# Kernel tuning notes

Measured on AMD Instinct MI355X. Metric: run time of the kernel, lower is better.

Reference implementation:

```python
import jax, jax.numpy as jnp
import numpy as np

T, B, M, H, NH = 4, 8, 1024, 768, 12
HD = H // NH
KMAX = 10


def _ln(x, s, b):
    mu = x.mean(-1, keepdims=True)
    var = ((x - mu) ** 2).mean(-1, keepdims=True)
    return (x - mu) * jax.lax.rsqrt(var + 1e-5) * s + b


def setup_inputs() -> dict:
    key = jax.random.key(0)
    ks = jax.random.split(key, 10)
    init = lambda k, shp: jax.random.normal(k, shp, jnp.float32) * 0.02
    return {
        'x': jax.random.normal(ks[0], (B, M, H), jnp.float32),
        'overlap': jax.random.randint(ks[1], (B, M, M), 0, KMAX + 1, jnp.int32),
        'lp': -jax.random.uniform(ks[2], (B, M), jnp.float32) * 10.0,
        'ln1_s': jnp.ones((T, H)), 'ln1_b': jnp.zeros((T, H)),
        'Wqkv': init(ks[3], (T, H, 3 * H)),
        'Wout': init(ks[4], (T, H, H)), 'bout': jnp.zeros((T, H)),
        'ln2_s': jnp.ones((T, H)), 'ln2_b': jnp.zeros((T, H)),
        'W1': init(ks[5], (T, H, 4 * H)), 'b1': jnp.zeros((T, 4 * H)),
        'W2': init(ks[6], (T, 4 * H, H)), 'b2': jnp.zeros((T, H)),
        'lno_s': jnp.ones((H,)), 'lno_b': jnp.zeros((H,)),
        'ov_emb': init(ks[7], (KMAX + 1,)),
        'ht_alpha': jnp.ones((1,), jnp.float32),
    }


def reference(x, overlap, lp, ln1_s, ln1_b, Wqkv, Wout, bout, ln2_s, ln2_b,
              W1, b1, W2, b2, lno_s, lno_b, ov_emb, ht_alpha):
    lp_c = jnp.clip(lp, -30.0, 0.0)                      # [B,M]
    ov = ov_emb[jnp.minimum(overlap, KMAX)]              # [B,M,M]
    bias = (ov - ht_alpha[0] * lp_c[:, None, :])[:, None]  # [B,1,M,M]
    scale = 1.0 / jnp.sqrt(jnp.float32(HD))
    for t in range(T):
        r = _ln(x, ln1_s[t], ln1_b[t])
        q, k, v = jnp.split(r @ Wqkv[t], 3, axis=-1)
        q = q.reshape(B, M, NH, HD).transpose(0, 2, 1, 3)
        k = k.reshape(B, M, NH, HD).transpose(0, 2, 1, 3)
        v = v.reshape(B, M, NH, HD).transpose(0, 2, 1, 3)
        s = jnp.einsum('bhqd,bhkd->bhqk', q, k) * scale + bias
        a = jax.nn.softmax(s, axis=-1)
        o = jnp.einsum('bhqk,bhkd->bhqd', a, v).transpose(0, 2, 1, 3).reshape(B, M, H)
        x = x + o @ Wout[t] + bout[t]
        h = _ln(x, ln2_s[t], ln2_b[t])
        x = x + jax.nn.gelu(h @ W1[t] + b1[t], approximate=False) @ W2[t] + b2[t]
    x = _ln(x, lno_s, lno_b)
    w = jax.nn.softmax(-lp_c, axis=1)                    # HT weights over m tokens
    return jnp.einsum('bm,bmh->bh', w, x)
```

## Files before the change

kernel.cpp:

```cpp
#include <hip/hip_runtime.h>
#include <hip/hip_bf16.h>
#include <math.h>

#define TT 4
#define BB 8
#define MM 1024
#define HH 768
#define NHEAD 12
#define HDIM 64
#define NTOK 8192
#define H3 2304
#define H4 3072

typedef __attribute__((ext_vector_type(8))) short bf16x8;
typedef __attribute__((ext_vector_type(4))) float f32x4;
typedef __attribute__((ext_vector_type(4))) unsigned short u16x4;

#define GLOBAL_AS(p) ((const __attribute__((address_space(1))) void*)(p))
#define LDS_AS(p)    ((__attribute__((address_space(3))) void*)(p))

__device__ __forceinline__ unsigned short f2bf(float f) {
  union { float f; unsigned u; } v; v.f = f;
  unsigned r = v.u + 0x7fffu + ((v.u >> 16) & 1u);
  return (unsigned short)(r >> 16);
}

__device__ __forceinline__ float fast_exp2(float x) {
#if __has_builtin(__builtin_amdgcn_exp2f)
  return __builtin_amdgcn_exp2f(x);
#else
  return exp2f(x);
#endif
}

__device__ __forceinline__ f32x4 mfma16(bf16x8 a, bf16x8 b, f32x4 c) {
  return __builtin_amdgcn_mfma_f32_16x16x32_bf16(a, b, c, 0, 0, 0);
}

__device__ __forceinline__ float block_sum256(float v, float* sh) {
  #pragma unroll
  for (int off = 32; off > 0; off >>= 1) v += __shfl_down(v, off);
  if ((threadIdx.x & 63) == 0) sh[threadIdx.x >> 6] = v;
  __syncthreads();
  v = sh[0] + sh[1] + sh[2] + sh[3];
  __syncthreads();
  return v;
}

__device__ __forceinline__ float block_max256(float v, float* sh) {
  #pragma unroll
  for (int off = 32; off > 0; off >>= 1) v = fmaxf(v, __shfl_down(v, off));
  if ((threadIdx.x & 63) == 0) sh[threadIdx.x >> 6] = v;
  __syncthreads();
  v = fmaxf(fmaxf(sh[0], sh[1]), fmaxf(sh[2], sh[3]));
  __syncthreads();
  return v;
}

__global__ __launch_bounds__(256) void wconv_kernel(const float* __restrict__ W,
                                                    unsigned short* __restrict__ Wt,
                                                    int K, int N) {
  __shared__ float tile[32][33];
  const int n0 = blockIdx.x * 32, k0 = blockIdx.y * 32;
  const int tx = threadIdx.x, ty = threadIdx.y;
  #pragma unroll
  for (int j = 0; j < 4; j++)
    tile[ty + j*8][tx] = W[(size_t)(k0 + ty + j*8) * N + n0 + tx];
  __syncthreads();
  #pragma unroll
  for (int j = 0; j < 4; j++)
    Wt[(size_t)(n0 + ty + j*8) * K + k0 + tx] = f2bf(tile[tx][ty + j*8]);
}

__global__ __launch_bounds__(256) void ln_kernel(const float* __restrict__ x,
                                                 const float* __restrict__ s,
                                                 const float* __restrict__ b,
                                                 unsigned short* __restrict__ out) {
  __shared__ float sh[4];
  const int row = blockIdx.x;
  const int tid = threadIdx.x;
  const float* xr = x + (size_t)row * HH;
  float v[3];
  float sum = 0.f;
  #pragma unroll
  for (int j = 0; j < 3; j++) { v[j] = xr[tid + j*256]; sum += v[j]; }
  sum = block_sum256(sum, sh);
  const float mu = sum * (1.f/768.f);
  float ss = 0.f;
  #pragma unroll
  for (int j = 0; j < 3; j++) { float d = v[j] - mu; ss += d*d; }
  ss = block_sum256(ss, sh);
  const float rstd = rsqrtf(ss * (1.f/768.f) + 1e-5f);
  #pragma unroll
  for (int j = 0; j < 3; j++) {
    int col = tid + j*256;
    out[(size_t)row * HH + col] = f2bf((v[j]-mu)*rstd*s[col] + b[col]);
  }
}

template<int EPI>
__global__ __launch_bounds__(256) void gemm_kernel(const unsigned short* __restrict__ A,
                                                   const unsigned short* __restrict__ Bt,
                                                   unsigned short* __restrict__ outB,
                                                   float* __restrict__ outF,
                                                   const float* __restrict__ bias,
                                                   int Ng, int Kg, int nx) {
  __shared__ unsigned short a_lds[2][128*64];
  __shared__ unsigned short b_lds[2][128*64];
  const int tid = threadIdx.x;
  const int w = tid >> 6, l = tid & 63;
  const int nwg = gridDim.x;
  const int lin = blockIdx.x;
  const int L = (lin & 7) * (nwg >> 3) + (lin >> 3);
  const int m0 = (L / nx) * 128, n0 = (L % nx) * 128;

  const int wr = (w >> 1) * 64, wc = (w & 1) * 64;
  const int l15 = l & 15, lhi = l >> 4;
  const int srow = w*32 + (l >> 3);
  const int schunk = (l & 7) ^ (l >> 3);
  const int scol = schunk << 3;

  f32x4 acc[4][4] = {};
  const int nk = Kg >> 6;
  int cur = 0;

  #pragma unroll
  for (int i = 0; i < 4; i++) {
    const unsigned short* gsa = A  + (size_t)(m0 + srow + i*8)*Kg + scol;
    const unsigned short* gsb = Bt + (size_t)(n0 + srow + i*8)*Kg + scol;
    __builtin_amdgcn_global_load_lds(GLOBAL_AS(gsa), LDS_AS(&a_lds[0][w*2048 + i*512]), 16, 0, 0);
    __builtin_amdgcn_global_load_lds(GLOBAL_AS(gsb), LDS_AS(&b_lds[0][w*2048 + i*512]), 16, 0, 0);
  }
  __syncthreads();

  for (int t = 0; t < nk; t++) {
    if (t + 1 < nk) {
      const int ks = (t + 1) << 6;
      #pragma unroll
      for (int i = 0; i < 4; i++) {
        const unsigned short* gsa = A  + (size_t)(m0 + srow + i*8)*Kg + ks + scol;
        const unsigned short* gsb = Bt + (size_t)(n0 + srow + i*8)*Kg + ks + scol;
        __builtin_amdgcn_global_load_lds(GLOBAL_AS(gsa), LDS_AS(&a_lds[cur^1][w*2048 + i*512]), 16, 0, 0);
        __builtin_amdgcn_global_load_lds(GLOBAL_AS(gsb), LDS_AS(&b_lds[cur^1][w*2048 + i*512]), 16, 0, 0);
      }
    }
    const unsigned short* ab = &a_lds[cur][0];
    const unsigned short* bb = &b_lds[cur][0];
    #pragma unroll
    for (int kb = 0; kb < 2; kb++) {
      bf16x8 af[4], bfr[4];
      const int rc = (kb*4 + lhi) ^ (l15 & 7);
      #pragma unroll
      for (int rb = 0; rb < 4; rb++)
        af[rb] = *(const bf16x8*)&ab[(wr + rb*16 + l15)*64 + (rc << 3)];
      #pragma unroll
      for (int nb = 0; nb < 4; nb++)
        bfr[nb] = *(const bf16x8*)&bb[(wc + nb*16 + l15)*64 + (rc << 3)];
      #pragma unroll
      for (int rb = 0; rb < 4; rb++)
        #pragma unroll
        for (int nb = 0; nb < 4; nb++)
          acc[rb][nb] = mfma16(af[rb], bfr[nb], acc[rb][nb]);
    }
    __syncthreads();
    cur ^= 1;
  }

  const int lr = lhi << 2;
  #pragma unroll
  for (int rb = 0; rb < 4; rb++)
    #pragma unroll
    for (int nb = 0; nb < 4; nb++) {
      const int row = m0 + wr + rb*16 + lr;
      const int col = n0 + wc + nb*16 + l15;
      #pragma unroll
      for (int r = 0; r < 4; r++) {
        float v = acc[rb][nb][r];
        const size_t off = (size_t)(row + r)*Ng + col;
        if (EPI == 0) {
          outB[off] = f2bf(v);
        } else if (EPI == 1) {
          v += bias[col];
          v = 0.5f * v * (1.f + erff(v * 0.70710678118654752f));
          outB[off] = f2bf(v);
        } else {
          v += bias[col] + outF[off];
          outF[off] = v;
        }
      }
    }
}

__global__ __launch_bounds__(256) void biasprep_kernel(const int* __restrict__ overlap,
                                                       const float* __restrict__ lp,
                                                       const float* __restrict__ ov_emb,
                                                       const float* __restrict__ ht_alpha,
                                                       float* __restrict__ biasP) {
  __shared__ float oe[11];
  if (threadIdx.x < 11) oe[threadIdx.x] = ov_emb[threadIdx.x] * 1.44269504088896f;
  __syncthreads();
  const float aL = ht_alpha[0] * 1.44269504088896f;
  const size_t base = ((size_t)blockIdx.x * 256 + threadIdx.x) * 4;
  const int b = (int)(base >> 20);
  const int k0 = (int)(base & 1023);
  int4 ov = *(const int4*)&overlap[base];
  float4 lv = *(const float4*)&lp[b * MM + k0];
  float4 o4;
  {
    int t0 = ov.x < 10 ? ov.x : 10; float c0 = fminf(fmaxf(lv.x, -30.f), 0.f); o4.x = oe[t0] - aL*c0;
    int t1 = ov.y < 10 ? ov.y : 10; float c1 = fminf(fmaxf(lv.y, -30.f), 0.f); o4.y = oe[t1] - aL*c1;
    int t2 = ov.z < 10 ? ov.z : 10; float c2 = fminf(fmaxf(lv.z, -30.f), 0.f); o4.z = oe[t2] - aL*c2;
    int t3 = ov.w < 10 ? ov.w : 10; float c3 = fminf(fmaxf(lv.w, -30.f), 0.f); o4.w = oe[t3] - aL*c3;
  }
  *(float4*)&biasP[base] = o4;
}

__global__ __launch_bounds__(256) void attn_kernel(const unsigned short* __restrict__ qkv,
                                                   const float* __restrict__ biasP,
                                                   unsigned short* __restrict__ obuf) {
  __shared__ unsigned short k_lds[64*64];
  __shared__ unsigned short v_lds[64*64];
  __shared__ unsigned short pmat[4][32*64];

  const int tid = threadIdx.x;
  const int w = tid >> 6, l = tid & 63;
  const int lin = blockIdx.x;
  const int L = (lin & 7) * 96 + (lin >> 3);
  const int h = L % 12;
  const int qb = (L / 12) & 7;
  const int b = L / 96;
  const int q0w = qb*128 + w*32;
  const int l15 = l & 15, lhi = l >> 4;
  const float SC = 0.125f * 1.44269504088896f;

  bf16x8 qf[2][2];
  #pragma unroll
  for (int rb = 0; rb < 2; rb++)
    #pragma unroll
    for (int kb = 0; kb < 2; kb++)
      qf[rb][kb] = *(const bf16x8*)&qkv[(size_t)(b*MM + q0w + rb*16 + l15)*H3 + h*HDIM + kb*32 + lhi*8];

  const float* brow[2];
  #pragma unroll
  for (int rb = 0; rb < 2; rb++)
    brow[rb] = biasP + (size_t)(b*MM + q0w + rb*16 + l15) * MM;

  f32x4 oacc[4][2] = {};
  float mrow[2] = {-INFINITY, -INFINITY};
  float lrow[2] = {0.f, 0.f};

  for (int kt = 0; kt < 16; kt++) {
    const int kbase = kt * 64;
    #pragma unroll
    for (int i = 0; i < 2; i++) {
      int idx = i*256 + tid;
      int kr = idx >> 3;
      int dc = (idx & 7) << 3;
      const size_t rowoff = (size_t)(b*MM + kbase + kr)*H3 + h*HDIM + dc;
      bf16x8 kv = *(const bf16x8*)&qkv[rowoff + HH];
      bf16x8 vv = *(const bf16x8*)&qkv[rowoff + 2*HH];
      *(bf16x8*)&k_lds[kr*64 + (dc ^ ((kr & 7) << 3))] = kv;
      #pragma unroll
      for (int j = 0; j < 8; j++) {
        int key = ((((dc >> 3) & 7) ^ j) & 7) << 3;
        v_lds[(dc + j)*64 + (kr ^ key)] = (unsigned short)(short)vv[j];
      }
    }
    __syncthreads();

    f32x4 sacc[4][2] = {};
    #pragma unroll
    for (int kb = 0; kb < 2; kb++) {
      bf16x8 ak[4];
      #pragma unroll
      for (int nb = 0; nb < 4; nb++) {
        int n = nb*16 + l15;
        ak[nb] = *(const bf16x8*)&k_lds[n*64 + ((kb*32 + lhi*8) ^ ((n & 7) << 3))];
      }
      #pragma unroll
      for (int nb = 0; nb < 4; nb++)
        #pragma unroll
        for (int rb = 0; rb < 2; rb++)
          sacc[nb][rb] = mfma16(ak[nb], qf[rb][kb], sacc[nb][rb]);
    }

    #pragma unroll
    for (int nb = 0; nb < 4; nb++)
      #pragma unroll
      for (int rb = 0; rb < 2; rb++) {
        f32x4 b4 = *(const f32x4*)&brow[rb][kbase + nb*16 + lhi*4];
        #pragma unroll
        for (int r = 0; r < 4; r++)
          sacc[nb][rb][r] = fmaf(sacc[nb][rb][r], SC, b4[r]);
      }

    float corrf[2];
    #pragma unroll
    for (int rb = 0; rb < 2; rb++) {
      float pm = sacc[0][rb][0];
      #pragma unroll
      for (int nb = 0; nb < 4; nb++)
        #pragma unroll
        for (int r = 0; r < 4; r++)
          pm = fmaxf(pm, sacc[nb][rb][r]);
      pm = fmaxf(pm, __shfl_xor(pm, 16));
      pm = fmaxf(pm, __shfl_xor(pm, 32));
      const float mnew = fmaxf(mrow[rb], pm);
      const float corr = fast_exp2(mrow[rb] - mnew);
      float rs = 0.f;
      #pragma unroll
      for (int nb = 0; nb < 4; nb++)
        #pragma unroll
        for (int r = 0; r < 4; r++) {
          float p = fast_exp2(sacc[nb][rb][r] - mnew);
          sacc[nb][rb][r] = p;
          rs += p;
        }
      rs += __shfl_xor(rs, 16);
      rs += __shfl_xor(rs, 32);
      mrow[rb] = mnew;
      lrow[rb] = lrow[rb]*corr + rs;
      corrf[rb] = corr;
    }
    #pragma unroll
    for (int db = 0; db < 4; db++)
      #pragma unroll
      for (int rb = 0; rb < 2; rb++)
        #pragma unroll
        for (int r = 0; r < 4; r++)
          oacc[db][rb][r] *= corrf[rb];

    unsigned short* pw = &pmat[w][0];
    #pragma unroll
    for (int nb = 0; nb < 4; nb++)
      #pragma unroll
      for (int rb = 0; rb < 2; rb++) {
        u16x4 pk;
        #pragma unroll
        for (int r = 0; r < 4; r++) pk[r] = f2bf(sacc[nb][rb][r]);
        *(u16x4*)&pw[(rb*16 + l15)*64 + ((nb*16 + lhi*4) ^ ((l15 & 7) << 3))] = pk;
      }

    #pragma unroll
    for (int kb = 0; kb < 2; kb++) {
      bf16x8 pb[2];
      #pragma unroll
      for (int rb = 0; rb < 2; rb++)
        pb[rb] = *(const bf16x8*)&pw[(rb*16 + l15)*64 + ((kb*32 + lhi*8) ^ ((l15 & 7) << 3))];
      bf16x8 av[4];
      #pragma unroll
      for (int db = 0; db < 4; db++) {
        int d = db*16 + l15;
        int key = ((((d >> 3) & 7) ^ (d & 7)) & 7) << 3;
        av[db] = *(const bf16x8*)&v_lds[d*64 + ((kb*32 + lhi*8) ^ key)];
      }
      #pragma unroll
      for (int db = 0; db < 4; db++)
        #pragma unroll
        for (int rb = 0; rb < 2; rb++)
          oacc[db][rb] = mfma16(av[db], pb[rb], oacc[db][rb]);
    }
    __syncthreads();
  }

  float inv[2] = { 1.f / lrow[0], 1.f / lrow[1] };
  unsigned short* pw = &pmat[w][0];
  #pragma unroll
  for (int db = 0; db < 4; db++)
    #pragma unroll
    for (int rb = 0; rb < 2; rb++) {
      u16x4 pk;
      #pragma unroll
      for (int r = 0; r < 4; r++) pk[r] = f2bf(oacc[db][rb][r] * inv[rb]);
      *(u16x4*)&pw[(rb*16 + l15)*64 + ((db*16 + lhi*4) ^ ((l15 & 7) << 3))] = pk;
    }
  #pragma unroll
  for (int rep = 0; rep < 4; rep++) {
    int qq = rep*8 + (l >> 3);
    int d0 = (l & 7) << 3;
    bf16x8 vv = *(const bf16x8*)&pw[qq*64 + (d0 ^ ((qq & 7) << 3))];
    *(bf16x8*)&obuf[(size_t)(b*MM + q0w + qq)*HH + h*HDIM + d0] = vv;
  }
}

__global__ __launch_bounds__(256) void htw_kernel(const float* __restrict__ lp,
                                                  float* __restrict__ w_ht) {
  __shared__ float sh[4];
  const int b = blockIdx.x, tid = threadIdx.x;
  float vals[4];
  float mx = -INFINITY;
  #pragma unroll
  for (int j = 0; j < 4; j++) {
    float lv = lp[b*MM + tid + j*256];
    float lc = fminf(fmaxf(lv, -30.f), 0.f);
    vals[j] = -lc;
    mx = fmaxf(mx, vals[j]);
  }
  mx = block_max256(mx, sh);
  float se = 0.f;
  #pragma unroll
  for (int j = 0; j < 4; j++) { vals[j] = expf(vals[j] - mx); se += vals[j]; }
  se = block_sum256(se, sh);
  const float inv = 1.f / se;
  #pragma unroll
  for (int j = 0; j < 4; j++) w_ht[b*MM + tid + j*256] = vals[j] * inv;
}

__global__ __launch_bounds__(256) void final_partial_kernel(const float* __restrict__ xbuf,
                                                            const float* __restrict__ lno_s,
                                                            const float* __restrict__ lno_b,
                                                            const float* __restrict__ w_ht,
                                                            float* __restrict__ part) {
  __shared__ float sh[4];
  const int b = blockIdx.x >> 4;
  const int chunk = blockIdx.x & 15;
  const int tid = threadIdx.x;
  float acc[3] = {0.f, 0.f, 0.f};
  float sc[3], bc[3];
  #pragma unroll
  for (int j = 0; j < 3; j++) { sc[j] = lno_s[tid + j*256]; bc[j] = lno_b[tid + j*256]; }
  for (int rr = 0; rr < 64; rr++) {
    const int tok = b*MM + chunk*64 + rr;
    const float* xr = xbuf + (size_t)tok * HH;
    float v[3]; float sum = 0.f;
    #pragma unroll
    for (int j = 0; j < 3; j++) { v[j] = xr[tid + j*256]; sum += v[j]; }
    sum = block_sum256(sum, sh);
    const float mu = sum * (1.f/768.f);
    float ss = 0.f;
    #pragma unroll
    for (int j = 0; j < 3; j++) { float d = v[j] - mu; ss += d*d; }
    ss = block_sum256(ss, sh);
    const float rstd = rsqrtf(ss * (1.f/768.f) + 1e-5f);
    const float wgt = w_ht[b*MM + chunk*64 + rr];
    #pragma unroll
    for (int j = 0; j < 3; j++) acc[j] += wgt * ((v[j]-mu)*rstd*sc[j] + bc[j]);
  }
  #pragma unroll
  for (int j = 0; j < 3; j++) part[(size_t)blockIdx.x * HH + tid + j*256] = acc[j];
}

__global__ __launch_bounds__(256) void final_reduce_kernel(const float* __restrict__ part,
                                                           float* __restrict__ out) {
  const int b = blockIdx.x;
  const int col = blockIdx.y*256 + threadIdx.x;
  float s = 0.f;
  #pragma unroll
  for (int c = 0; c < 16; c++) s += part[(size_t)(b*16 + c) * HH + col];
  out[b*HH + col] = s;
}

extern "C" void kernel_launch(void* const* d_in, const int* in_sizes, int n_in,
                              void* d_out, int out_size, void* d_ws, size_t ws_size,
                              hipStream_t stream) {
  (void)in_sizes; (void)n_in; (void)ws_size;
  const float* x      = (const float*)d_in[0];
  const int*   overlap= (const int*)d_in[1];
  const float* lp     = (const float*)d_in[2];
  const float* ln1_s  = (const float*)d_in[3];
  const float* ln1_b  = (const float*)d_in[4];
  const float* Wqkv   = (const float*)d_in[5];
  const float* Wout   = (const float*)d_in[6];
  const float* bout   = (const float*)d_in[7];
  const float* ln2_s  = (const float*)d_in[8];
  const float* ln2_b  = (const float*)d_in[9];
  const float* W1     = (const float*)d_in[10];
  const float* b1     = (const float*)d_in[11];
  const float* W2     = (const float*)d_in[12];
  const float* b2     = (const float*)d_in[13];
  const float* lno_s  = (const float*)d_in[14];
  const float* lno_b  = (const float*)d_in[15];
  const float* ov_emb = (const float*)d_in[16];
  const float* ht_alpha = (const float*)d_in[17];
  float* out = (float*)d_out;

  char* ws = (char*)d_ws;
  float*          xbuf  = (float*)(ws + 0);
  unsigned short* lnout = (unsigned short*)(ws + 25165824);
  unsigned short* qkv   = (unsigned short*)(ws + 37748736);
  unsigned short* obuf  = (unsigned short*)(ws + 75497472);
  unsigned short* gbuf  = (unsigned short*)(ws + 88080384);
  unsigned short* wbuf  = (unsigned short*)(ws + 138412032);
  float*          w_ht  = (float*)(ws + 143130624);
  float*          part  = (float*)(ws + 143163392);
  float*          biasP = (float*)gbuf;

  hipMemcpyAsync(xbuf, x, (size_t)NTOK * HH * sizeof(float), hipMemcpyDeviceToDevice, stream);
  htw_kernel<<<BB, 256, 0, stream>>>(lp, w_ht);

  for (int t = 0; t < TT; t++) {
    wconv_kernel<<<dim3(H3/32, HH/32), dim3(32, 8), 0, stream>>>(Wqkv + (size_t)t*HH*H3, wbuf, HH, H3);
    ln_kernel<<<NTOK, 256, 0, stream>>>(xbuf, ln1_s + t*HH, ln1_b + t*HH, lnout);
    gemm_kernel<0><<<(H3/128)*(NTOK/128), 256, 0, stream>>>(lnout, wbuf, qkv, nullptr, nullptr, H3, HH, H3/128);
    biasprep_kernel<<<(BB*MM*MM/4)/256, 256, 0, stream>>>(overlap, lp, ov_emb, ht_alpha, biasP);
    attn_kernel<<<BB*NHEAD*(MM/128), 256, 0, stream>>>(qkv, biasP, obuf);
    wconv_kernel<<<dim3(HH/32, HH/32), dim3(32, 8), 0, stream>>>(Wout + (size_t)t*HH*HH, wbuf, HH, HH);
    gemm_kernel<2><<<(HH/128)*(NTOK/128), 256, 0, stream>>>(obuf, wbuf, nullptr, xbuf, bout + t*HH, HH, HH, HH/128);
    ln_kernel<<<NTOK, 256, 0, stream>>>(xbuf, ln2_s + t*HH, ln2_b + t*HH, lnout);
    wconv_kernel<<<dim3(H4/32, HH/32), dim3(32, 8), 0, stream>>>(W1 + (size_t)t*HH*H4, wbuf, HH, H4);
    gemm_kernel<1><<<(H4/128)*(NTOK/128), 256, 0, stream>>>(lnout, wbuf, gbuf, nullptr, b1 + t*H4, H4, HH, H4/128);
    wconv_kernel<<<dim3(HH/32, H4/32), dim3(32, 8), 0, stream>>>(W2 + (size_t)t*H4*HH, wbuf, H4, HH);
    gemm_kernel<2><<<(HH/128)*(NTOK/128), 256, 0, stream>>>(gbuf, wbuf, nullptr, xbuf, b2 + t*HH, HH, H4, HH/128);
  }

  final_partial_kernel<<<BB*16, 256, 0, stream>>>(xbuf, lno_s, lno_b, w_ht, part);
  final_reduce_kernel<<<dim3(BB, 3), 256, 0, stream>>>(part, out);

  (void)out_size;
}
```

Before: 1.504 ms.

## Double-buffer attention K/V, defer softmax rescale, tanh GELU, hoist bias prep

Attention now double-buffers K/V in LDS, prefetching the next tile (K via direct global-to-LDS loads) while the current tile computes, and raises wave priority around the MFMA blocks. It also skips the output rescale when the running max grows by at most 8, the exact-erf GELU becomes a tanh approximation built on exp2, and the attention bias is built once in spare workspace instead of once per layer. Together these target load latency in attention, transcendental cost in the FC1 epilogue, and three redundant bias passes, at the cost of more LDS, an extra barrier per tile, and a GELU that differs slightly from the exact-erf reference.

```diff
diff --git a/kernel.cpp b/kernel.cpp
--- a/kernel.cpp
+++ b/kernel.cpp
@@ -181,7 +181,11 @@
           outB[off] = f2bf(v);
         } else if (EPI == 1) {
           v += bias[col];
-          v = 0.5f * v * (1.f + erff(v * 0.70710678118654752f));
+          float u = 0.79788456080287f * v * (1.f + 0.044715f * v * v);
+          u = fminf(u, 15.f);
+          float e = fast_exp2(u * 2.88539008177793f);
+          float th = 1.f - 2.f / (e + 1.f);
+          v = 0.5f * v * (1.f + th);
           outB[off] = f2bf(v);
         } else {
           v += bias[col] + outF[off];
@@ -218,8 +222,8 @@
 __global__ __launch_bounds__(256) void attn_kernel(const unsigned short* __restrict__ qkv,
                                                    const float* __restrict__ biasP,
                                                    unsigned short* __restrict__ obuf) {
-  __shared__ unsigned short k_lds[64*64];
-  __shared__ unsigned short v_lds[64*64];
+  __shared__ unsigned short k_lds[2][64*64];
+  __shared__ unsigned short v_lds[2][64*64];
   __shared__ unsigned short pmat[4][32*64];
 
   const int tid = threadIdx.x;
@@ -233,6 +237,10 @@
   const int l15 = l & 15, lhi = l >> 4;
   const float SC = 0.125f * 1.44269504088896f;
 
+  const int kr_s = l >> 3;
+  const int schunk = (l & 7) ^ kr_s;
+  const int dc = (l & 7) << 3;
+
   bf16x8 qf[2][2];
   #pragma unroll
   for (int rb = 0; rb < 2; rb++)
@@ -249,33 +257,55 @@
   float mrow[2] = {-INFINITY, -INFINITY};
   float lrow[2] = {0.f, 0.f};
 
+
+  {
+    #pragma unroll
+    for (int i = 0; i < 2; i++) {
+      const unsigned short* g = qkv + (size_t)(b*MM + 0 + i*32 + w*8 + kr_s)*H3 + h*HDIM + HH + schunk*8;
+      __builtin_amdgcn_global_load_lds(GLOBAL_AS(g), LDS_AS(&k_lds[0][(i*32 + w*8)*64]), 16, 0, 0);
+    }
+    bf16x8 vr[2];
+    #pragma unroll
+    for (int i = 0; i < 2; i++)
+      vr[i] = *(const bf16x8*)&qkv[(size_t)(b*MM + 0 + i*32 + w*8 + kr_s)*H3 + h*HDIM + 2*HH + dc];
+    #pragma unroll
+    for (int i = 0; i < 2; i++) {
+      int kr = i*32 + w*8 + kr_s;
+      #pragma unroll
+      for (int j = 0; j < 8; j++) {
+        int key = ((((dc >> 3) & 7) ^ j) & 7) << 3;
+        v_lds[0][(dc + j)*64 + (kr ^ key)] = (unsigned short)(short)vr[i][j];
+      }
+    }
+    __syncthreads();
+  }
+
+  int cur = 0;
   for (int kt = 0; kt < 16; kt++) {
     const int kbase = kt * 64;
-    #pragma unroll
-    for (int i = 0; i < 2; i++) {
-      int idx = i*256 + tid;
-      int kr = idx >> 3;
-      int dc = (idx & 7) << 3;
-      const size_t rowoff = (size_t)(b*MM + kbase + kr)*H3 + h*HDIM + dc;
-      bf16x8 kv = *(const bf16x8*)&qkv[rowoff + HH];
-      bf16x8 vv = *(const bf16x8*)&qkv[rowoff + 2*HH];
-      *(bf16x8*)&k_lds[kr*64 + (dc ^ ((kr & 7) << 3))] = kv;
-      #pragma unroll
-      for (int j = 0; j < 8; j++) {
-        int key = ((((dc >> 3) & 7) ^ j) & 7) << 3;
-        v_lds[(dc + j)*64 + (kr ^ key)] = (unsigned short)(short)vv[j];
-      }
-    }
-    __syncthreads();
+    bf16x8 vrN[2];
+    if (kt < 15) {
+      const int nbase = kbase + 64;
+      #pragma unroll
+      for (int i = 0; i < 2; i++) {
+        const unsigned short* g = qkv + (size_t)(b*MM + nbase + i*32 + w*8 + kr_s)*H3 + h*HDIM + HH + schunk*8;
+        __builtin_amdgcn_global_load_lds(GLOBAL_AS(g), LDS_AS(&k_lds[cur^1][(i*32 + w*8)*64]), 16, 0, 0);
+      }
+      #pragma unroll
+      for (int i = 0; i < 2; i++)
+        vrN[i] = *(const bf16x8*)&qkv[(size_t)(b*MM + nbase + i*32 + w*8 + kr_s)*H3 + h*HDIM + 2*HH + dc];
+    }
 
     f32x4 sacc[4][2] = {};
+    const unsigned short* kb_lds = &k_lds[cur][0];
+    __builtin_amdgcn_s_setprio(1);
     #pragma unroll
     for (int kb = 0; kb < 2; kb++) {
       bf16x8 ak[4];
       #pragma unroll
       for (int nb = 0; nb < 4; nb++) {
         int n = nb*16 + l15;
-        ak[nb] = *(const bf16x8*)&k_lds[n*64 + ((kb*32 + lhi*8) ^ ((n & 7) << 3))];
+        ak[nb] = *(const bf16x8*)&kb_lds[n*64 + ((kb*32 + lhi*8) ^ ((n & 7) << 3))];
       }
       #pragma unroll
       for (int nb = 0; nb < 4; nb++)
@@ -283,6 +313,7 @@
         for (int rb = 0; rb < 2; rb++)
           sacc[nb][rb] = mfma16(ak[nb], qf[rb][kb], sacc[nb][rb]);
     }
+    __builtin_amdgcn_s_setprio(0);
 
     #pragma unroll
     for (int nb = 0; nb < 4; nb++)
@@ -295,6 +326,7 @@
       }
 
     float corrf[2];
+    int defer[2];
     #pragma unroll
     for (int rb = 0; rb < 2; rb++) {
       float pm = sacc[0][rb][0];
@@ -305,8 +337,9 @@
           pm = fmaxf(pm, sacc[nb][rb][r]);
       pm = fmaxf(pm, __shfl_xor(pm, 16));
       pm = fmaxf(pm, __shfl_xor(pm, 32));
-      const float mnew = fmaxf(mrow[rb], pm);
-      const float corr = fast_exp2(mrow[rb] - mnew);
+      defer[rb] = __all(pm - mrow[rb] <= 8.0f);
+      const float mnew = defer[rb] ? mrow[rb] : fmaxf(mrow[rb], pm);
+      const float corr = defer[rb] ? 1.0f : fast_exp2(mrow[rb] - mnew);
       float rs = 0.f;
       #pragma unroll
       for (int nb = 0; nb < 4; nb++)
@@ -323,12 +356,14 @@
       corrf[rb] = corr;
     }
     #pragma unroll
-    for (int db = 0; db < 4; db++)
-      #pragma unroll
-      for (int rb = 0; rb < 2; rb++)
-        #pragma unroll
-        for (int r = 0; r < 4; r++)
-          oacc[db][rb][r] *= corrf[rb];
+    for (int rb = 0; rb < 2; rb++)
+      if (!defer[rb]) {
+        #pragma unroll
+        for (int db = 0; db < 4; db++)
+          #pragma unroll
+          for (int r = 0; r < 4; r++)
+            oacc[db][rb][r] *= corrf[rb];
+      }
 
     unsigned short* pw = &pmat[w][0];
     #pragma unroll
@@ -341,6 +376,8 @@
         *(u16x4*)&pw[(rb*16 + l15)*64 + ((nb*16 + lhi*4) ^ ((l15 & 7) << 3))] = pk;
       }
 
+    const unsigned short* vb_lds = &v_lds[cur][0];
+    __builtin_amdgcn_s_setprio(1);
     #pragma unroll
     for (int kb = 0; kb < 2; kb++) {
       bf16x8 pb[2];
@@ -352,7 +389,7 @@
       for (int db = 0; db < 4; db++) {
         int d = db*16 + l15;
         int key = ((((d >> 3) & 7) ^ (d & 7)) & 7) << 3;
-        av[db] = *(const bf16x8*)&v_lds[d*64 + ((kb*32 + lhi*8) ^ key)];
+        av[db] = *(const bf16x8*)&vb_lds[d*64 + ((kb*32 + lhi*8) ^ key)];
       }
       #pragma unroll
       for (int db = 0; db < 4; db++)
@@ -360,7 +397,22 @@
         for (int rb = 0; rb < 2; rb++)
           oacc[db][rb] = mfma16(av[db], pb[rb], oacc[db][rb]);
     }
+    __builtin_amdgcn_s_setprio(0);
+
     __syncthreads();
+    if (kt < 15) {
+      #pragma unroll
+      for (int i = 0; i < 2; i++) {
+        int kr = i*32 + w*8 + kr_s;
+        #pragma unroll
+        for (int j = 0; j < 8; j++) {
+          int key = ((((dc >> 3) & 7) ^ j) & 7) << 3;
+          v_lds[cur^1][(dc + j)*64 + (kr ^ key)] = (unsigned short)(short)vrN[i][j];
+        }
+      }
+    }
+    __syncthreads();
+    cur ^= 1;
   }
 
   float inv[2] = { 1.f / lrow[0], 1.f / lrow[1] };
@@ -453,7 +505,7 @@
 extern "C" void kernel_launch(void* const* d_in, const int* in_sizes, int n_in,
                               void* d_out, int out_size, void* d_ws, size_t ws_size,
                               hipStream_t stream) {
-  (void)in_sizes; (void)n_in; (void)ws_size;
+  (void)in_sizes; (void)n_in;
   const float* x      = (const float*)d_in[0];
   const int*   overlap= (const int*)d_in[1];
   const float* lp     = (const float*)d_in[2];
@@ -483,16 +535,20 @@
   unsigned short* wbuf  = (unsigned short*)(ws + 138412032);
   float*          w_ht  = (float*)(ws + 143130624);
   float*          part  = (float*)(ws + 143163392);
-  float*          biasP = (float*)gbuf;
+  const int prep_once = (ws_size >= (size_t)143556608 + (size_t)33554432);
+  float*          biasP = prep_once ? (float*)(ws + 143556608) : (float*)gbuf;
 
   hipMemcpyAsync(xbuf, x, (size_t)NTOK * HH * sizeof(float), hipMemcpyDeviceToDevice, stream);
   htw_kernel<<<BB, 256, 0, stream>>>(lp, w_ht);
+  if (prep_once)
+    biasprep_kernel<<<(BB*MM*MM/4)/256, 256, 0, stream>>>(overlap, lp, ov_emb, ht_alpha, biasP);
 
   for (int t = 0; t < TT; t++) {
     wconv_kernel<<<dim3(H3/32, HH/32), dim3(32, 8), 0, stream>>>(Wqkv + (size_t)t*HH*H3, wbuf, HH, H3);
     ln_kernel<<<NTOK, 256, 0, stream>>>(xbuf, ln1_s + t*HH, ln1_b + t*HH, lnout);
     gemm_kernel<0><<<(H3/128)*(NTOK/128), 256, 0, stream>>>(lnout, wbuf, qkv, nullptr, nullptr, H3, HH, H3/128);
-    biasprep_kernel<<<(BB*MM*MM/4)/256, 256, 0, stream>>>(overlap, lp, ov_emb, ht_alpha, biasP);
+    if (!prep_once)
+      biasprep_kernel<<<(BB*MM*MM/4)/256, 256, 0, stream>>>(overlap, lp, ov_emb, ht_alpha, biasP);
     attn_kernel<<<BB*NHEAD*(MM/128), 256, 0, stream>>>(qkv, biasP, obuf);
     wconv_kernel<<<dim3(HH/32, HH/32), dim3(32, 8), 0, stream>>>(Wout + (size_t)t*HH*HH, wbuf, HH, HH);
     gemm_kernel<2><<<(HH/128)*(NTOK/128), 256, 0, stream>>>(obuf, wbuf, nullptr, xbuf, bout + t*HH, HH, HH, HH/128);
```

Result: faster. 1.443 ms (-4.1%).
